# Kernel tuning notes

Hardware: AMD Instinct MI355X
Metric: run time of the kernel (lower is better)

## Reference

```python
import jax, jax.numpy as jnp
import numpy as np

N = 50000      # nodes
E = 800000     # edges (avg degree 16)
DIN = 128      # input_dim
DH = 128       # hidden_dim
H = 8          # num_heads
DK = DH // H   # 16
TN = 8         # num_node_types
TE = 8         # num_edge_types
NB = 4         # num_bases


def setup_inputs() -> dict:
    key = jax.random.key(0)
    ks = jax.random.split(key, 20)
    inp = {}
    inp['node_feat'] = jax.random.normal(ks[0], (N, DIN), jnp.float32)
    inp['node_type'] = jax.random.randint(ks[1], (N,), 0, TN)
    inp['src'] = jax.random.randint(ks[2], (E,), 0, N)
    inp['dst'] = jax.random.randint(ks[3], (E,), 0, N)
    inp['edge_type'] = jax.random.randint(ks[4], (E,), 0, TE)
    s = 0.05
    for i, nm in enumerate(['k', 'q', 'v', 'a']):
        inp['w_comp_' + nm] = jax.random.normal(ks[5 + 2 * i], (TN, NB), jnp.float32) * s
        inp['w_basis_' + nm] = jax.random.normal(ks[6 + 2 * i], (NB, DIN * DH), jnp.float32) * s
    inp['relation_pri'] = jnp.ones((TE, H), jnp.float32)
    inp['relation_att'] = jax.random.uniform(ks[13], (TE, H, DK, DK), jnp.float32, -0.25, 0.25)
    inp['relation_msg'] = jax.random.uniform(ks[14], (TE, H, DK, DK), jnp.float32, -0.25, 0.25)
    inp['loop_weight'] = jax.random.uniform(ks[15], (DIN, DH), jnp.float32, -0.08, 0.08)
    inp['bias'] = jnp.zeros((DH,), jnp.float32)
    return inp


def _decomp(x, nt, w_comp, w_basis):
    # basis regularizer: per-node-type weight W[t] = sum_b w_comp[t,b] * basis[b]
    T = w_comp.shape[0]
    W = (w_comp @ w_basis).reshape(T, x.shape[-1], -1)   # [T, in, out]
    h_all = jnp.einsum('ni,tio->tno', x, W)              # [T, N, out]
    return h_all[nt, jnp.arange(x.shape[0])]             # gather per-node type


def reference(node_feat, node_type, src, dst, edge_type,
              w_comp_k, w_basis_k, w_comp_q, w_basis_q,
              w_comp_v, w_basis_v, w_comp_a, w_basis_a,
              relation_pri, relation_att, relation_msg, loop_weight, bias):
    n = node_feat.shape[0]
    scale = (DH / H) ** -0.5
    # node init: k/q/v projections (per-node-type basis transforms)
    k = _decomp(node_feat, node_type, w_comp_k, w_basis_k).reshape(n, H, DK)
    q = _decomp(node_feat, node_type, w_comp_q, w_basis_q).reshape(n, H, DK)
    v = _decomp(node_feat, node_type, w_comp_v, w_basis_v).reshape(n, H, DK)
    # edge init: HGT attention. kt = k[src] @ relation_att[etype], computed
    # per-type at node granularity then gathered (avoids [E,H,dk,dk] gather).
    kt = jnp.einsum('nhi,thij->tnhj', k, relation_att)[edge_type, src]   # [E,H,dk]
    e = (q[dst] * kt).sum(-1) * relation_pri[edge_type] * scale          # [E,H]
    # edge softmax over incoming edges of each dst node
    m = jax.ops.segment_max(e, dst, num_segments=n)
    ex = jnp.exp(e - m[dst])
    denom = jax.ops.segment_sum(ex, dst, num_segments=n)
    a = ex / denom[dst]                                                  # [E,H]
    # message: v[src] @ relation_msg[etype], weighted by attention, sum-reduce
    vt = jnp.einsum('nhi,thij->tnhj', v, relation_msg)[edge_type, src]   # [E,H,dk]
    agg = jax.ops.segment_sum(a[..., None] * vt, dst, num_segments=n)    # [N,H,dk]
    agg = agg.reshape(n, DH)
    # node update: a_transform + self loop + bias + relu (dropout=0, no BN)
    out = _decomp(agg, node_type, w_comp_a, w_basis_a)
    out = out + node_feat @ loop_weight + bias
    return jax.nn.relu(out)
```

## Files before the change

### kernel.cpp

```cpp
#include <hip/hip_runtime.h>
#include <hip/hip_bf16.h>
#include <stdint.h>

#define DIN 128
#define DHID 128
#define TN 8
#define TE 8
#define NBASE 4

typedef short s8v __attribute__((ext_vector_type(8)));
typedef float f4v __attribute__((ext_vector_type(4)));

static __device__ __forceinline__ float bf2f(__hip_bfloat16 x){ return __bfloat162float(x); }
static __device__ __forceinline__ float lo16f(uint32_t u){ return __builtin_bit_cast(float, u << 16); }
static __device__ __forceinline__ float hi16f(uint32_t u){ return __builtin_bit_cast(float, u & 0xFFFF0000u); }
static __device__ __forceinline__ uint16_t f2bfu(float x){ return __builtin_bit_cast(uint16_t, __float2bfloat16(x)); }
static __device__ __forceinline__ uint32_t packbf2(float lo, float hi){
    return (uint32_t)f2bfu(lo) | ((uint32_t)f2bfu(hi) << 16);
}
static __device__ __forceinline__ float ldf(const void* p, int i, int flag){
    return flag ? ((const float*)p)[i] : bf2f(((const __hip_bfloat16*)p)[i]);
}
static __device__ __forceinline__ int imin(int a, int b){ return a < b ? a : b; }
template<int CTRL>
static __device__ __forceinline__ float dpp_add(float x){
    int xi = __builtin_bit_cast(int, x);
    int yi = __builtin_amdgcn_update_dpp(xi, xi, CTRL, 0xF, 0xF, true);
    return x + __builtin_bit_cast(float, yi);
}

__global__ void k_prep(const int* __restrict__ dst, const int* __restrict__ etv, int E,
                       const int* __restrict__ ntype, int Nn,
                       const void* __restrict__ xin,
                       const void* __restrict__ ck, const void* __restrict__ bk,
                       const void* __restrict__ cq, const void* __restrict__ bq,
                       const void* __restrict__ cv, const void* __restrict__ bv,
                       const void* __restrict__ ca, const void* __restrict__ ba,
                       const void* __restrict__ lw, const void* __restrict__ rpri,
                       const void* __restrict__ ratt, const void* __restrict__ rmsg,
                       int* __restrict__ deg8, int* __restrict__ tcount,
                       uint32_t* __restrict__ xbf,
                       __hip_bfloat16* __restrict__ WkqvT, __hip_bfloat16* __restrict__ WfinT,
                       uint32_t* __restrict__ Apk, uint32_t* __restrict__ Mpk,
                       int* __restrict__ dflag)
{
    int flag = (((const uint32_t*)rpri)[0] == 0x3F803F80u) ? 0 : 1;
    __shared__ int lt[TN];
    if (threadIdx.x < TN) lt[threadIdx.x] = 0;
    __syncthreads();
    int gid = blockIdx.x * 256 + threadIdx.x;
    int stride = gridDim.x * 256;
    if (gid == 0) dflag[0] = flag;
    const int NW = Nn * 64;
    const int T3 = TN * 3 * 128 * 128;
    const int T4 = TN * 128 * 256;
    for (int e = gid; e < E; e += stride)
        atomicAdd(&deg8[dst[e] * 8 + etv[e]], 1);
    for (int n = gid; n < Nn; n += stride)
        atomicAdd(&lt[ntype[n]], 1);
    if (flag) {
        const float2* f = (const float2*)xin;
        for (int w = gid; w < NW; w += stride) { float2 v = f[w]; xbf[w] = packbf2(v.x, v.y); }
    } else {
        const uint32_t* s = (const uint32_t*)xin;
        for (int w = gid; w < NW; w += stride) xbf[w] = s[w];
    }
    for (int idx = gid; idx < T3; idx += stride) {
        int t = idx / 49152; int r = idx % 49152;
        int proj = r / 16384; int r2 = r % 16384;
        int j = r2 >> 7; int i = r2 & 127;
        const void* c = (proj == 0) ? ck : ((proj == 1) ? cq : cv);
        const void* b = (proj == 0) ? bk : ((proj == 1) ? bq : bv);
        float s = 0.f;
        #pragma unroll
        for (int bb = 0; bb < NBASE; ++bb)
            s += ldf(c, t * NBASE + bb, flag) * ldf(b, bb * 16384 + i * 128 + j, flag);
        WkqvT[idx] = __float2bfloat16(s);
    }
    for (int r = gid; r < T4; r += stride) {
        int t = r >> 15; int r2 = r & 32767;
        int j = r2 >> 8; int kk = r2 & 255;
        float s;
        if (kk < 128) {
            s = 0.f;
            #pragma unroll
            for (int bb = 0; bb < NBASE; ++bb)
                s += ldf(ca, t * NBASE + bb, flag) * ldf(ba, bb * 16384 + kk * 128 + j, flag);
        } else {
            s = ldf(lw, (kk - 128) * 128 + j, flag);
        }
        WfinT[r] = __float2bfloat16(s);
    }
    for (int w = gid; w < 8192; w += stride) {
        int eh = w >> 7, blk = (w >> 3) & 15, p = w & 7;
        float ps = ldf(rpri, eh, flag) * 0.25f;
        float a0 = ldf(ratt, (eh * 16 + blk) * 16 + 2 * p, flag) * ps;
        float a1 = ldf(ratt, (eh * 16 + blk) * 16 + 2 * p + 1, flag) * ps;
        Apk[w] = packbf2(a0, a1);
        float m0 = ldf(rmsg, (eh * 16 + 2 * p) * 16 + blk, flag);
        float m1 = ldf(rmsg, (eh * 16 + 2 * p + 1) * 16 + blk, flag);
        Mpk[w] = packbf2(m0, m1);
    }
    __syncthreads();
    if (threadIdx.x < TN) atomicAdd(&tcount[threadIdx.x], lt[threadIdx.x]);
}

__global__ void __launch_bounds__(1024) k_scanA(const int* __restrict__ deg8, int n,
                                                int* __restrict__ bsum)
{
    __shared__ int ws[16];
    int i = blockIdx.x * 1024 + threadIdx.x;
    int v = (i < n) ? deg8[i] : 0;
    #pragma unroll
    for (int o = 1; o < 64; o <<= 1) v += __shfl_xor(v, o, 64);
    int lane = threadIdx.x & 63, wv = threadIdx.x >> 6;
    if (lane == 0) ws[wv] = v;
    __syncthreads();
    if (threadIdx.x == 0) {
        int s = 0;
        #pragma unroll
        for (int w = 0; w < 16; ++w) s += ws[w];
        bsum[blockIdx.x] = s;
    }
}

__global__ void __launch_bounds__(512) k_scanB(int* __restrict__ bsum, int nblk,
                                               const int* __restrict__ tcount,
                                               int* __restrict__ toff, int* __restrict__ tcur)
{
    __shared__ int ws[8];
    int t = threadIdx.x;
    int v = (t < nblk) ? bsum[t] : 0;
    int lane = t & 63, wv = t >> 6;
    int sc = v;
    #pragma unroll
    for (int o = 1; o < 64; o <<= 1) { int tt = __shfl_up(sc, o, 64); if (lane >= o) sc += tt; }
    if (lane == 63) ws[wv] = sc;
    __syncthreads();
    int wb = 0;
    for (int w = 0; w < wv; ++w) wb += ws[w];
    if (t < nblk) bsum[t] = wb + sc - v;
    if (t == 0) {
        int s = 0;
        for (int k = 0; k < TN; ++k) { toff[k] = s; tcur[k] = s; s += tcount[k]; }
        toff[TN] = s;
    }
}

__global__ void __launch_bounds__(1024) k_scanC(const int* __restrict__ deg8, int n,
                                                const int* __restrict__ bsum,
                                                int* __restrict__ eoff8, int* __restrict__ ecur8,
                                                int E)
{
    __shared__ int ws[16];
    int i = blockIdx.x * 1024 + threadIdx.x;
    int v = (i < n) ? deg8[i] : 0;
    int lane = threadIdx.x & 63, wv = threadIdx.x >> 6;
    int sc = v;
    #pragma unroll
    for (int o = 1; o < 64; o <<= 1) { int tt = __shfl_up(sc, o, 64); if (lane >= o) sc += tt; }
    if (lane == 63) ws[wv] = sc;
    __syncthreads();
    int wb = bsum[blockIdx.x];
    for (int w = 0; w < wv; ++w) wb += ws[w];
    int ex = wb + sc - v;
    if (i < n) { eoff8[i] = ex; ecur8[i] = ex; }
    if (i == 0) eoff8[n] = E;
}

__global__ void k_scatter(const int* __restrict__ src, const int* __restrict__ dst,
                          const int* __restrict__ etv, int E,
                          const int* __restrict__ ntype, int Nn,
                          int* __restrict__ ecur8, int* __restrict__ esrc,
                          int* __restrict__ tcur, int* __restrict__ perm)
{
    int stride = gridDim.x * blockDim.x;
    int i0 = blockIdx.x * blockDim.x + threadIdx.x;
    for (int e = i0; e < E; e += stride) {
        int p = atomicAdd(&ecur8[dst[e] * 8 + etv[e]], 1);
        esrc[p] = src[e];
    }
    for (int n = i0; n < Nn; n += stride) {
        int p = atomicAdd(&tcur[ntype[n]], 1);
        perm[p] = n;
    }
}

__global__ void __launch_bounds__(256, 2) k_proj(
    const __hip_bfloat16* __restrict__ xbf,
    const __hip_bfloat16* __restrict__ WkqvT,
    const int* __restrict__ perm, const int* __restrict__ ntype,
    uint32_t* __restrict__ kv, __hip_bfloat16* __restrict__ q16, int Nn)
{
    int lane = threadIdx.x & 63;
    int wave = blockIdx.x * 4 + (threadIdx.x >> 6);
    int row0 = wave * 32;
    if (row0 >= Nn) return;
    int col = lane & 15, quad = lane >> 4;
    int anode[2], onode[2][4], otype[2][4];
    #pragma unroll
    for (int s = 0; s < 2; ++s) {
        int r0 = row0 + s * 16;
        int ar = r0 + col;
        anode[s] = perm[(ar < Nn) ? ar : (Nn - 1)];
        #pragma unroll
        for (int r = 0; r < 4; ++r) {
            int oi = r0 + quad * 4 + r;
            bool v = (oi < Nn);
            onode[s][r] = perm[v ? oi : (Nn - 1)];
            otype[s][r] = v ? ntype[onode[s][r]] : -1;
        }
    }
    int tfirst = ntype[perm[row0]];
    int lastI = row0 + 31; if (lastI >= Nn) lastI = Nn - 1;
    int tlast = ntype[perm[lastI]];
    const s8v* arow0 = (const s8v*)(xbf + (size_t)anode[0] * DIN);
    const s8v* arow1 = (const s8v*)(xbf + (size_t)anode[1] * DIN);
    for (int t = tfirst; t <= tlast; ++t) {
        #pragma unroll 1
        for (int proj = 0; proj < 3; ++proj) {
            f4v acc[2][8];
            #pragma unroll
            for (int s = 0; s < 2; ++s)
                #pragma unroll
                for (int nb = 0; nb < 8; ++nb) acc[s][nb] = (f4v){0.f, 0.f, 0.f, 0.f};
            const __hip_bfloat16* bb = WkqvT + (size_t)t * 49152 + proj * 16384;
            #pragma unroll
            for (int kq = 0; kq < 4; ++kq) {
                s8v a0 = arow0[kq * 4 + quad];
                s8v a1 = arow1[kq * 4 + quad];
                #pragma unroll
                for (int nb = 0; nb < 8; ++nb) {
                    int J = nb * 16 + col;
                    s8v b = *((const s8v*)(bb + (size_t)J * 128) + (kq * 4 + quad));
                    acc[0][nb] = __builtin_amdgcn_mfma_f32_16x16x32_bf16(a0, b, acc[0][nb], 0, 0, 0);
                    acc[1][nb] = __builtin_amdgcn_mfma_f32_16x16x32_bf16(a1, b, acc[1][nb], 0, 0, 0);
                }
            }
            #pragma unroll
            for (int s = 0; s < 2; ++s)
            #pragma unroll
            for (int nb = 0; nb < 8; ++nb) {
                int jj = nb * 16 + col;
                #pragma unroll
                for (int r = 0; r < 4; ++r) {
                    if (otype[s][r] == t) {
                        uint16_t hv = f2bfu(acc[s][nb][r]);
                        size_t node = (size_t)onode[s][r];
                        if (proj == 0)      ((uint16_t*)kv)[node * 256 + jj] = hv;
                        else if (proj == 1) ((uint16_t*)q16)[node * 128 + jj] = hv;
                        else                ((uint16_t*)kv)[node * 256 + 128 + jj] = hv;
                    }
                }
            }
        }
    }
}

__global__ void __launch_bounds__(256, 4) k_edge(
    const uint32_t* __restrict__ kvp, const uint32_t* __restrict__ qp,
    const uint32_t* __restrict__ Apk, const uint32_t* __restrict__ Mpk,
    const int* __restrict__ eoff8, const int* __restrict__ esrc,
    uint32_t* __restrict__ agg, int Nn)
{
    __shared__ float sS[4][164];
    int tid = threadIdx.x, lane = tid & 63, wv = tid >> 6;
    int h = lane >> 3, x = lane & 7;
    float* Srow = &sS[wv][h * 20];
    int wid = blockIdx.x * 4 + wv;
    int nw = gridDim.x * 4;
    for (int n = wid; n < Nn; n += nw) {
        int pb = n * 8;
        int P0 = eoff8[pb];
        int P1 = eoff8[pb + 8];
        if (P0 >= P1) { agg[(size_t)n * 64 + lane] = 0u; continue; }
        int c1 = P1 - 1;
        int s0 = esrc[P0];
        int s1 = esrc[imin(P0 + 1, c1)];
        int s2 = esrc[imin(P0 + 2, c1)];
        int s3 = esrc[imin(P0 + 3, c1)];
        uint32_t kb0 = kvp[(size_t)s0 * 128 + lane], vb0 = kvp[(size_t)s0 * 128 + 64 + lane];
        uint32_t kb1 = kvp[(size_t)s1 * 128 + lane], vb1 = kvp[(size_t)s1 * 128 + 64 + lane];
        uint32_t kb2 = kvp[(size_t)s2 * 128 + lane], vb2 = kvp[(size_t)s2 * 128 + 64 + lane];
        uint32_t kb3 = kvp[(size_t)s3 * 128 + lane], vb3 = kvp[(size_t)s3 * 128 + 64 + lane];
        int sn0 = esrc[imin(P0 + 4, c1)];
        int sn1 = esrc[imin(P0 + 5, c1)];
        int sn2 = esrc[imin(P0 + 6, c1)];
        int sn3 = esrc[imin(P0 + 7, c1)];
        int pk = P0 + 4, ps = P0 + 8;
        const uint4* qb = (const uint4*)(qp + (size_t)n * 64 + h * 8);
        uint4 qw0 = qb[0], qw1 = qb[1];
        uint32_t qarr[8] = {qw0.x, qw0.y, qw0.z, qw0.w, qw1.x, qw1.y, qw1.z, qw1.w};
        float qv[16];
        #pragma unroll
        for (int p = 0; p < 8; ++p) { qv[2 * p] = lo16f(qarr[p]); qv[2 * p + 1] = hi16f(qarr[p]); }
        float l = 0.f, T0 = 0.f, T1 = 0.f;
        int pnext = P0;
        #pragma unroll 1
        for (int et = 0; et < 8; ++et) {
            int p0 = pnext;
            pnext = eoff8[pb + et + 1];
            int p1r = pnext;
            if (p0 >= p1r) continue;
            const uint4* Ab = (const uint4*)(Apk + (((et * 8 + h) * 16 + 2 * x) * 8));
            uint4 A0 = Ab[0], A1 = Ab[1], A2 = Ab[2], A3 = Ab[3];
            uint32_t aw[16] = {A0.x, A0.y, A0.z, A0.w, A1.x, A1.y, A1.z, A1.w,
                               A2.x, A2.y, A2.z, A2.w, A3.x, A3.y, A3.z, A3.w};
            float qA0 = 0.f, qA1 = 0.f;
            #pragma unroll
            for (int p = 0; p < 8; ++p) {
                qA0 = fmaf(lo16f(aw[p]), qv[2 * p], qA0);
                qA0 = fmaf(hi16f(aw[p]), qv[2 * p + 1], qA0);
                qA1 = fmaf(lo16f(aw[8 + p]), qv[2 * p], qA1);
                qA1 = fmaf(hi16f(aw[8 + p]), qv[2 * p + 1], qA1);
            }
            float S0 = 0.f, S1 = 0.f;
            for (int p = p0; p < p1r; ++p) {
                uint32_t kc = kb0, vc = vb0;
                kb0 = kb1; vb0 = vb1; kb1 = kb2; vb1 = vb2; kb2 = kb3; vb2 = vb3;
                if (pk < P1) {
                    kb3 = kvp[(size_t)sn0 * 128 + lane];
                    vb3 = kvp[(size_t)sn0 * 128 + 64 + lane];
                }
                ++pk;
                sn0 = sn1; sn1 = sn2; sn2 = sn3;
                sn3 = esrc[(ps < P1) ? ps : c1];
                ++ps;
                float ep = fmaf(hi16f(kc), qA1, lo16f(kc) * qA0);
                ep = dpp_add<0xB1>(ep);
                ep = dpp_add<0x4E>(ep);
                ep = dpp_add<0x141>(ep);
                float exv = __expf(ep);
                l += exv;
                S0 = fmaf(exv, lo16f(vc), S0);
                S1 = fmaf(exv, hi16f(vc), S1);
            }
            float2 st; st.x = S0; st.y = S1;
            *(float2*)&Srow[2 * x] = st;
            float4 sv0 = *(const float4*)&Srow[0];
            float4 sv1 = *(const float4*)&Srow[4];
            float4 sv2 = *(const float4*)&Srow[8];
            float4 sv3 = *(const float4*)&Srow[12];
            float Sv[16] = {sv0.x, sv0.y, sv0.z, sv0.w, sv1.x, sv1.y, sv1.z, sv1.w,
                            sv2.x, sv2.y, sv2.z, sv2.w, sv3.x, sv3.y, sv3.z, sv3.w};
            const uint4* Mb = (const uint4*)(Mpk + (((et * 8 + h) * 16 + 2 * x) * 8));
            uint4 M0 = Mb[0], M1 = Mb[1], M2 = Mb[2], M3 = Mb[3];
            uint32_t mw[16] = {M0.x, M0.y, M0.z, M0.w, M1.x, M1.y, M1.z, M1.w,
                               M2.x, M2.y, M2.z, M2.w, M3.x, M3.y, M3.z, M3.w};
            #pragma unroll
            for (int p = 0; p < 8; ++p) {
                T0 = fmaf(lo16f(mw[p]), Sv[2 * p], T0);
                T0 = fmaf(hi16f(mw[p]), Sv[2 * p + 1], T0);
                T1 = fmaf(lo16f(mw[8 + p]), Sv[2 * p], T1);
                T1 = fmaf(hi16f(mw[8 + p]), Sv[2 * p + 1], T1);
            }
        }
        float inv = (l > 0.f) ? (1.f / l) : 0.f;
        agg[(size_t)n * 64 + lane] = packbf2(T0 * inv, T1 * inv);
    }
}

__global__ void __launch_bounds__(256, 2) k_final(
    const __hip_bfloat16* __restrict__ xbf,
    const __hip_bfloat16* __restrict__ aggbf,
    const __hip_bfloat16* __restrict__ WfinT,
    const void* __restrict__ bias,
    const int* __restrict__ perm, const int* __restrict__ ntype,
    void* __restrict__ outv, int Nn, const int* __restrict__ dflag)
{
    int flag = dflag[0];
    int lane = threadIdx.x & 63;
    int wave = blockIdx.x * 4 + (threadIdx.x >> 6);
    int row0 = wave * 32;
    if (row0 >= Nn) return;
    int col = lane & 15, quad = lane >> 4;
    int anode[2], onode[2][4], otype[2][4];
    #pragma unroll
    for (int s = 0; s < 2; ++s) {
        int r0 = row0 + s * 16;
        int ar = r0 + col;
        anode[s] = perm[(ar < Nn) ? ar : (Nn - 1)];
        #pragma unroll
        for (int r = 0; r < 4; ++r) {
            int oi = r0 + quad * 4 + r;
            bool v = (oi < Nn);
            onode[s][r] = perm[v ? oi : (Nn - 1)];
            otype[s][r] = v ? ntype[onode[s][r]] : -1;
        }
    }
    int tfirst = ntype[perm[row0]];
    int lastI = row0 + 31; if (lastI >= Nn) lastI = Nn - 1;
    int tlast = ntype[perm[lastI]];
    const s8v* ag0 = (const s8v*)(aggbf + (size_t)anode[0] * DHID);
    const s8v* ag1 = (const s8v*)(aggbf + (size_t)anode[1] * DHID);
    const s8v* ax0 = (const s8v*)(xbf + (size_t)anode[0] * DIN);
    const s8v* ax1 = (const s8v*)(xbf + (size_t)anode[1] * DIN);
    for (int t = tfirst; t <= tlast; ++t) {
        f4v acc[2][8];
        #pragma unroll
        for (int s = 0; s < 2; ++s)
            #pragma unroll
            for (int nb = 0; nb < 8; ++nb) acc[s][nb] = (f4v){0.f, 0.f, 0.f, 0.f};
        const __hip_bfloat16* bbase = WfinT + (size_t)t * 32768;
        #pragma unroll
        for (int kq = 0; kq < 8; ++kq) {
            s8v a0 = (kq < 4) ? ag0[kq * 4 + quad] : ax0[(kq - 4) * 4 + quad];
            s8v a1 = (kq < 4) ? ag1[kq * 4 + quad] : ax1[(kq - 4) * 4 + quad];
            #pragma unroll
            for (int nb = 0; nb < 8; ++nb) {
                int J = nb * 16 + col;
                s8v b = *((const s8v*)(bbase + (size_t)J * 256) + (kq * 4 + quad));
                acc[0][nb] = __builtin_amdgcn_mfma_f32_16x16x32_bf16(a0, b, acc[0][nb], 0, 0, 0);
                acc[1][nb] = __builtin_amdgcn_mfma_f32_16x16x32_bf16(a1, b, acc[1][nb], 0, 0, 0);
            }
        }
        #pragma unroll
        for (int s = 0; s < 2; ++s)
        #pragma unroll
        for (int nb = 0; nb < 8; ++nb) {
            int J = nb * 16 + col;
            float bj = ldf(bias, J, flag);
            #pragma unroll
            for (int r = 0; r < 4; ++r) {
                if (otype[s][r] == t) {
                    float val = fmaxf(acc[s][nb][r] + bj, 0.f);
                    size_t oi = (size_t)onode[s][r] * DHID + J;
                    if (flag) ((float*)outv)[oi] = val;
                    else ((__hip_bfloat16*)outv)[oi] = __float2bfloat16(val);
                }
            }
        }
    }
}

extern "C" void kernel_launch(void* const* d_in, const int* in_sizes, int n_in,
                              void* d_out, int out_size, void* d_ws, size_t ws_size,
                              hipStream_t stream)
{
    const void* xfeat = d_in[0];
    const int* ntype = (const int*)d_in[1];
    const int* srcv  = (const int*)d_in[2];
    const int* dstv  = (const int*)d_in[3];
    const int* etypv = (const int*)d_in[4];
    const void* ck = d_in[5];
    const void* bk = d_in[6];
    const void* cq = d_in[7];
    const void* bq = d_in[8];
    const void* cv = d_in[9];
    const void* bv = d_in[10];
    const void* ca = d_in[11];
    const void* ba = d_in[12];
    const void* rpri = d_in[13];
    const void* ratt = d_in[14];
    const void* rmsg = d_in[15];
    const void* lw   = d_in[16];
    const void* bias = d_in[17];
    int Nn = in_sizes[1];
    int E  = in_sizes[2];

    char* w = (char*)d_ws;
    size_t off = 0;
    auto alloc = [&](size_t b) -> char* {
        char* r = w + off;
        off = (off + b + 255) & ~(size_t)255;
        return r;
    };
    __hip_bfloat16* WkqvT = (__hip_bfloat16*)alloc((size_t)TN * 3 * 128 * 128 * 2);
    __hip_bfloat16* WfinT = (__hip_bfloat16*)alloc((size_t)TN * 256 * 128 * 2);
    __hip_bfloat16* xbf = (__hip_bfloat16*)alloc((size_t)Nn * 128 * 2);
    uint32_t* kv = (uint32_t*)alloc((size_t)Nn * 128 * 4);
    __hip_bfloat16* q16 = (__hip_bfloat16*)alloc((size_t)Nn * 128 * 2);
    __hip_bfloat16* aggbf = (__hip_bfloat16*)alloc((size_t)Nn * 128 * 2);
    uint32_t* Apk = (uint32_t*)alloc(8192 * 4);
    uint32_t* Mpk = (uint32_t*)alloc(8192 * 4);
    int n8 = Nn * 8;
    int* deg8   = (int*)alloc((size_t)(n8 + TN) * 4);
    int* tcount = deg8 + n8;
    int* eoff8  = (int*)alloc((size_t)(n8 + 1) * 4);
    int* ecur8  = (int*)alloc((size_t)n8 * 4);
    int nblk = (n8 + 1023) / 1024;
    int* bsum   = (int*)alloc((size_t)(nblk + 8) * 4);
    int* toff   = (int*)alloc((TN + 1) * 4);
    int* tcur   = (int*)alloc(TN * 4);
    int* perm   = (int*)alloc((size_t)Nn * 4);
    int* esrc   = (int*)alloc((size_t)E * 4);
    int* dflag  = (int*)alloc(4);

    hipMemsetAsync(deg8, 0, (size_t)(n8 + TN) * 4, stream);
    k_prep<<<2048, 256, 0, stream>>>(dstv, etypv, E, ntype, Nn, xfeat,
                                     ck, bk, cq, bq, cv, bv, ca, ba, lw, rpri, ratt, rmsg,
                                     deg8, tcount, (uint32_t*)xbf, WkqvT, WfinT, Apk, Mpk, dflag);
    k_scanA<<<nblk, 1024, 0, stream>>>(deg8, n8, bsum);
    k_scanB<<<1, 512, 0, stream>>>(bsum, nblk, tcount, toff, tcur);
    k_scanC<<<nblk, 1024, 0, stream>>>(deg8, n8, bsum, eoff8, ecur8, E);
    k_scatter<<<2048, 256, 0, stream>>>(srcv, dstv, etypv, E, ntype, Nn, ecur8, esrc, tcur, perm);
    int stiles = (Nn + 31) / 32;
    int pblocks = (stiles + 3) / 4;
    k_proj<<<pblocks, 256, 0, stream>>>(xbf, WkqvT, perm, ntype, kv, q16, Nn);
    k_edge<<<2048, 256, 0, stream>>>(kv, (const uint32_t*)q16, Apk, Mpk, eoff8, esrc,
                                     (uint32_t*)aggbf, Nn);
    k_final<<<pblocks, 256, 0, stream>>>(xbf, aggbf, WfinT, bias, perm, ntype,
                                         d_out, Nn, dflag);
}
```

Baseline: 705.5 us.

## Interleave K/V per lane for single 8-byte gathers and raise edge-kernel occupancy

The projection kernel now writes K and V interleaved per bf16 pair, so each lane's K word and V word sit next to each other. The edge kernel can then fetch both with one 8-byte load per source node instead of two separate 4-byte loads. Launch bounds for the edge kernel go from 4 to 8 blocks per SM. The A/M relation-matrix loads are split into two halves to lower register pressure so that target is reachable. The added occupancy is meant to hide the latency of the irregular gathers, at the risk of register spills.

```diff
diff --git a/kernel.cpp b/kernel.cpp
--- a/kernel.cpp
+++ b/kernel.cpp
@@ -247,9 +247,10 @@
                     if (otype[s][r] == t) {
                         uint16_t hv = f2bfu(acc[s][nb][r]);
                         size_t node = (size_t)onode[s][r];
-                        if (proj == 0)      ((uint16_t*)kv)[node * 256 + jj] = hv;
+                        int l2 = jj >> 1, half = jj & 1;
+                        if (proj == 0)      ((uint16_t*)kv)[node * 256 + l2 * 4 + half] = hv;
                         else if (proj == 1) ((uint16_t*)q16)[node * 128 + jj] = hv;
-                        else                ((uint16_t*)kv)[node * 256 + 128 + jj] = hv;
+                        else                ((uint16_t*)kv)[node * 256 + l2 * 4 + 2 + half] = hv;
                     }
                 }
             }
@@ -257,7 +258,7 @@
     }
 }
 
-__global__ void __launch_bounds__(256, 4) k_edge(
+__global__ void __launch_bounds__(256, 8) k_edge(
     const uint32_t* __restrict__ kvp, const uint32_t* __restrict__ qp,
     const uint32_t* __restrict__ Apk, const uint32_t* __restrict__ Mpk,
     const int* __restrict__ eoff8, const int* __restrict__ esrc,
@@ -267,6 +268,7 @@
     int tid = threadIdx.x, lane = tid & 63, wv = tid >> 6;
     int h = lane >> 3, x = lane & 7;
     float* Srow = &sS[wv][h * 20];
+    const uint2* kvi = (const uint2*)kvp;
     int wid = blockIdx.x * 4 + wv;
     int nw = gridDim.x * 4;
     for (int n = wid; n < Nn; n += nw) {
@@ -279,10 +281,10 @@
         int s1 = esrc[imin(P0 + 1, c1)];
         int s2 = esrc[imin(P0 + 2, c1)];
         int s3 = esrc[imin(P0 + 3, c1)];
-        uint32_t kb0 = kvp[(size_t)s0 * 128 + lane], vb0 = kvp[(size_t)s0 * 128 + 64 + lane];
-        uint32_t kb1 = kvp[(size_t)s1 * 128 + lane], vb1 = kvp[(size_t)s1 * 128 + 64 + lane];
-        uint32_t kb2 = kvp[(size_t)s2 * 128 + lane], vb2 = kvp[(size_t)s2 * 128 + 64 + lane];
-        uint32_t kb3 = kvp[(size_t)s3 * 128 + lane], vb3 = kvp[(size_t)s3 * 128 + 64 + lane];
+        uint2 b0 = kvi[(size_t)s0 * 64 + lane];
+        uint2 b1 = kvi[(size_t)s1 * 64 + lane];
+        uint2 b2 = kvi[(size_t)s2 * 64 + lane];
+        uint2 b3 = kvi[(size_t)s3 * 64 + lane];
         int sn0 = esrc[imin(P0 + 4, c1)];
         int sn1 = esrc[imin(P0 + 5, c1)];
         int sn2 = esrc[imin(P0 + 6, c1)];
@@ -303,37 +305,42 @@
             int p1r = pnext;
             if (p0 >= p1r) continue;
             const uint4* Ab = (const uint4*)(Apk + (((et * 8 + h) * 16 + 2 * x) * 8));
-            uint4 A0 = Ab[0], A1 = Ab[1], A2 = Ab[2], A3 = Ab[3];
-            uint32_t aw[16] = {A0.x, A0.y, A0.z, A0.w, A1.x, A1.y, A1.z, A1.w,
-                               A2.x, A2.y, A2.z, A2.w, A3.x, A3.y, A3.z, A3.w};
             float qA0 = 0.f, qA1 = 0.f;
-            #pragma unroll
-            for (int p = 0; p < 8; ++p) {
-                qA0 = fmaf(lo16f(aw[p]), qv[2 * p], qA0);
-                qA0 = fmaf(hi16f(aw[p]), qv[2 * p + 1], qA0);
-                qA1 = fmaf(lo16f(aw[8 + p]), qv[2 * p], qA1);
-                qA1 = fmaf(hi16f(aw[8 + p]), qv[2 * p + 1], qA1);
+            {
+                uint4 A0 = Ab[0], A1 = Ab[1];
+                uint32_t aw[8] = {A0.x, A0.y, A0.z, A0.w, A1.x, A1.y, A1.z, A1.w};
+                #pragma unroll
+                for (int p = 0; p < 8; ++p) {
+                    qA0 = fmaf(lo16f(aw[p]), qv[2 * p], qA0);
+                    qA0 = fmaf(hi16f(aw[p]), qv[2 * p + 1], qA0);
+                }
+            }
+            {
+                uint4 A2 = Ab[2], A3 = Ab[3];
+                uint32_t aw[8] = {A2.x, A2.y, A2.z, A2.w, A3.x, A3.y, A3.z, A3.w};
+                #pragma unroll
+                for (int p = 0; p < 8; ++p) {
+                    qA1 = fmaf(lo16f(aw[p]), qv[2 * p], qA1);
+                    qA1 = fmaf(hi16f(aw[p]), qv[2 * p + 1], qA1);
+                }
             }
             float S0 = 0.f, S1 = 0.f;
             for (int p = p0; p < p1r; ++p) {
-                uint32_t kc = kb0, vc = vb0;
-                kb0 = kb1; vb0 = vb1; kb1 = kb2; vb1 = vb2; kb2 = kb3; vb2 = vb3;
-                if (pk < P1) {
-                    kb3 = kvp[(size_t)sn0 * 128 + lane];
-                    vb3 = kvp[(size_t)sn0 * 128 + 64 + lane];
-                }
+                uint2 c = b0;
+                b0 = b1; b1 = b2; b2 = b3;
+                if (pk < P1) b3 = kvi[(size_t)sn0 * 64 + lane];
                 ++pk;
                 sn0 = sn1; sn1 = sn2; sn2 = sn3;
                 sn3 = esrc[(ps < P1) ? ps : c1];
                 ++ps;
-                float ep = fmaf(hi16f(kc), qA1, lo16f(kc) * qA0);
+                float ep = fmaf(hi16f(c.x), qA1, lo16f(c.x) * qA0);
                 ep = dpp_add<0xB1>(ep);
                 ep = dpp_add<0x4E>(ep);
                 ep = dpp_add<0x141>(ep);
                 float exv = __expf(ep);
                 l += exv;
-                S0 = fmaf(exv, lo16f(vc), S0);
-                S1 = fmaf(exv, hi16f(vc), S1);
+                S0 = fmaf(exv, lo16f(c.y), S0);
+                S1 = fmaf(exv, hi16f(c.y), S1);
             }
             float2 st; st.x = S0; st.y = S1;
             *(float2*)&Srow[2 * x] = st;
@@ -344,15 +351,23 @@
             float Sv[16] = {sv0.x, sv0.y, sv0.z, sv0.w, sv1.x, sv1.y, sv1.z, sv1.w,
                             sv2.x, sv2.y, sv2.z, sv2.w, sv3.x, sv3.y, sv3.z, sv3.w};
             const uint4* Mb = (const uint4*)(Mpk + (((et * 8 + h) * 16 + 2 * x) * 8));
-            uint4 M0 = Mb[0], M1 = Mb[1], M2 = Mb[2], M3 = Mb[3];
-            uint32_t mw[16] = {M0.x, M0.y, M0.z, M0.w, M1.x, M1.y, M1.z, M1.w,
-                               M2.x, M2.y, M2.z, M2.w, M3.x, M3.y, M3.z, M3.w};
-            #pragma unroll
-            for (int p = 0; p < 8; ++p) {
-                T0 = fmaf(lo16f(mw[p]), Sv[2 * p], T0);
-                T0 = fmaf(hi16f(mw[p]), Sv[2 * p + 1], T0);
-                T1 = fmaf(lo16f(mw[8 + p]), Sv[2 * p], T1);
-                T1 = fmaf(hi16f(mw[8 + p]), Sv[2 * p + 1], T1);
+            {
+                uint4 M0 = Mb[0], M1 = Mb[1];
+                uint32_t mw[8] = {M0.x, M0.y, M0.z, M0.w, M1.x, M1.y, M1.z, M1.w};
+                #pragma unroll
+                for (int p = 0; p < 8; ++p) {
+                    T0 = fmaf(lo16f(mw[p]), Sv[2 * p], T0);
+                    T0 = fmaf(hi16f(mw[p]), Sv[2 * p + 1], T0);
+                }
+            }
+            {
+                uint4 M2 = Mb[2], M3 = Mb[3];
+                uint32_t mw[8] = {M2.x, M2.y, M2.z, M2.w, M3.x, M3.y, M3.z, M3.w};
+                #pragma unroll
+                for (int p = 0; p < 8; ++p) {
+                    T1 = fmaf(lo16f(mw[p]), Sv[2 * p], T1);
+                    T1 = fmaf(hi16f(mw[p]), Sv[2 * p + 1], T1);
+                }
             }
         }
         float inv = (l > 0.f) ? (1.f / l) : 0.f;
```

New measurement: 851.7 us. 20.7% more time.
